# Performance work log

Hardware: AMD Instinct MI355X
Metric: run time of the kernel (lower is better)

## Reference

```python
import jax, jax.numpy as jnp
import numpy as np

Q7_MAX = 127.0  # int8 symmetric quant range
EPS = 1e-8


def setup_inputs() -> dict:
    key = jax.random.key(0)
    k0, k1, k2, k3 = jax.random.split(key, 4)
    tokens, d_in, d_out = 4096, 4096, 6144  # 32*128 + 8*128 + 8*128
    x = jax.random.normal(k0, (tokens, d_in), dtype=jnp.float32)
    # pre-quantized int8 weight [out_features, in_features]
    weight = jax.random.randint(k1, (d_out, d_in), -128, 128, dtype=jnp.int8)
    # per-output-channel dequant scale [out_features, 1]
    scale = jax.random.uniform(k2, (d_out, 1), dtype=jnp.float32, minval=1e-3, maxval=1e-2)
    bias = jax.random.normal(k3, (d_out,), dtype=jnp.float32) * 0.01
    return {"x": x, "weight": weight, "scale": scale, "bias": bias}


def reference(x, weight, scale, bias):
    # dynamic per-token symmetric int8 quantization of activations
    amax = jnp.max(jnp.abs(x), axis=-1, keepdims=True)          # [T, 1]
    s_x = jnp.maximum(amax, EPS) / Q7_MAX                        # per-token scale
    x_q = jnp.clip(jnp.round(x / s_x), -128.0, 127.0).astype(jnp.int8)
    acc = jnp.matmul(x_q.astype(jnp.int32), weight.astype(jnp.int32).T)
    # fused dequant: per-token act scale * per-channel weight scale, plus bias
    out = acc.astype(jnp.float32) * s_x * scale.T + bias
    return out
```

## Files before the change

kernel.cpp:

```cpp
#include <hip/hip_runtime.h>
#include <stdint.h>
#include <stddef.h>

typedef __attribute__((ext_vector_type(4))) int i32x4;

#define AS1q __attribute__((address_space(1)))
#define AS3q __attribute__((address_space(3)))

__device__ __forceinline__ void gload16(const void* g, void* l) {
    __builtin_amdgcn_global_load_lds((const AS1q uint32_t*)g, (AS3q uint32_t*)l, 16, 0, 0);
}

#define VMCNT(n)  asm volatile("s_waitcnt vmcnt(" #n ")" ::: "memory")
#define BARRIER() asm volatile("s_barrier" ::: "memory")

#define EPSQ 1e-8f

__global__ __launch_bounds__(256) void quant4096(
    const float* __restrict__ x, int8_t* __restrict__ xq, float* __restrict__ sx)
{
    constexpr int K = 4096;
    const int t = blockIdx.x;
    const int tid = threadIdx.x;
    const float4* row4 = (const float4*)(x + (size_t)t * K);
    float4 v0 = row4[0 * 256 + tid];
    float4 v1 = row4[1 * 256 + tid];
    float4 v2 = row4[2 * 256 + tid];
    float4 v3 = row4[3 * 256 + tid];
    auto mx4 = [](float4 a) {
        return fmaxf(fmaxf(fabsf(a.x), fabsf(a.y)), fmaxf(fabsf(a.z), fabsf(a.w)));
    };
    float am = fmaxf(fmaxf(mx4(v0), mx4(v1)), fmaxf(mx4(v2), mx4(v3)));
    #pragma unroll
    for (int off = 32; off > 0; off >>= 1)
        am = fmaxf(am, __shfl_xor(am, off, 64));
    __shared__ float wmax[4];
    if ((tid & 63) == 0) wmax[tid >> 6] = am;
    __syncthreads();
    float r = fmaxf(fmaxf(wmax[0], wmax[1]), fmaxf(wmax[2], wmax[3]));
    const float s = fmaxf(r, EPSQ) / 127.0f;
    if (tid == 0) sx[t] = s;
    int* qrow = (int*)(xq + (size_t)t * K);
    auto pack = [&](float4 a) {
        int q0 = (int)fminf(fmaxf(rintf(a.x / s), -128.f), 127.f);
        int q1 = (int)fminf(fmaxf(rintf(a.y / s), -128.f), 127.f);
        int q2 = (int)fminf(fmaxf(rintf(a.z / s), -128.f), 127.f);
        int q3 = (int)fminf(fmaxf(rintf(a.w / s), -128.f), 127.f);
        return (q0 & 255) | ((q1 & 255) << 8) | ((q2 & 255) << 16) | ((q3 & 255) << 24);
    };
    qrow[0 * 256 + tid] = pack(v0);
    qrow[1 * 256 + tid] = pack(v1);
    qrow[2 * 256 + tid] = pack(v2);
    qrow[3 * 256 + tid] = pack(v3);
}

__global__ __launch_bounds__(256) void quant_any(
    const float* __restrict__ x, int8_t* __restrict__ xq, float* __restrict__ sx, int K)
{
    const int t = blockIdx.x;
    const int tid = threadIdx.x;
    const float* row = x + (size_t)t * K;
    float am = 0.f;
    for (int i = tid; i < K; i += 256) am = fmaxf(am, fabsf(row[i]));
    #pragma unroll
    for (int off = 32; off > 0; off >>= 1)
        am = fmaxf(am, __shfl_xor(am, off, 64));
    __shared__ float wmax[4];
    if ((tid & 63) == 0) wmax[tid >> 6] = am;
    __syncthreads();
    float r = fmaxf(fmaxf(wmax[0], wmax[1]), fmaxf(wmax[2], wmax[3]));
    const float s = fmaxf(r, EPSQ) / 127.0f;
    if (tid == 0) sx[t] = s;
    int8_t* qrow = xq + (size_t)t * K;
    for (int i = tid; i < K; i += 256) {
        float q = fminf(fmaxf(rintf(row[i] / s), -128.f), 127.f);
        qrow[i] = (int8_t)(int)q;
    }
}

__global__ __launch_bounds__(256) void pack_w(
    const int* __restrict__ w32, int8_t* __restrict__ w8, long long n4)
{
    const long long stride = (long long)gridDim.x * 256;
    for (long long i = (long long)blockIdx.x * 256 + threadIdx.x; i < n4; i += stride) {
        int4 v = ((const int4*)w32)[i];
        ((int*)w8)[i] = (v.x & 255) | ((v.y & 255) << 8) | ((v.z & 255) << 16) | ((v.w & 255) << 24);
    }
}

__global__ __launch_bounds__(256, 2) void gemm_i8(
    const int8_t* __restrict__ xq, const int8_t* __restrict__ w,
    const float* __restrict__ sx, const float* __restrict__ scale,
    const float* __restrict__ bias, float* __restrict__ out,
    int M, int N, int K)
{
    __shared__ __align__(16) uint8_t lds[2][24576];
    const int tid  = threadIdx.x;
    const int lane = tid & 63;
    const int wv   = tid >> 6;
    const int wr   = wv >> 1, wc = wv & 1;

    const int nwg = gridDim.x;
    const int q8 = nwg >> 3, r8 = nwg & 7;
    const int xcd = blockIdx.x & 7, idx8 = blockIdx.x >> 3;
    const int wg = (xcd < r8 ? xcd * (q8 + 1) : r8 * (q8 + 1) + (xcd - r8) * q8) + idx8;

    const int NBM = M >> 8;
    const int bm = wg % NBM;
    const int bn = wg / NBM;
    const int brow = bm << 8, bcol = bn << 7;

    const int8_t* srcA[4];
    const int8_t* srcB[2];
    #pragma unroll
    for (int e = 0; e < 4; ++e) {
        int li = e * 256 + tid;
        int R  = li >> 3;
        int x  = ((li & 7) << 4) ^ ((R & 7) << 4);
        srcA[e] = xq + (size_t)(brow + ((R << 1) | (x >> 6))) * K + (x & 63);
    }
    #pragma unroll
    for (int e = 0; e < 2; ++e) {
        int li = e * 256 + tid;
        int R  = li >> 3;
        int x  = ((li & 7) << 4) ^ ((R & 7) << 4);
        srcB[e] = w + (size_t)(bcol + ((R << 1) | (x >> 6))) * K + (x & 63);
    }

    int offA[8], offB[4];
    #pragma unroll
    for (int m = 0; m < 8; ++m) {
        int r  = wr * 128 + m * 16 + (lane & 15);
        int R  = r >> 1;
        int x  = (((r & 1) << 6) | (lane & 48)) ^ ((R & 7) << 4);
        offA[m] = R * 128 + x;
    }
    #pragma unroll
    for (int n = 0; n < 4; ++n) {
        int r  = wc * 64 + n * 16 + (lane & 15);
        int R  = r >> 1;
        int x  = (((r & 1) << 6) | (lane & 48)) ^ ((R & 7) << 4);
        offB[n] = 16384 + R * 128 + x;
    }

    i32x4 acc[8][4] = {};

    auto stage = [&](int buf, int kt) {
        const size_t ko = (size_t)kt << 6;
        #pragma unroll
        for (int e = 0; e < 4; ++e)
            gload16(srcA[e] + ko, &lds[buf][e * 4096 + wv * 1024]);
        #pragma unroll
        for (int e = 0; e < 2; ++e)
            gload16(srcB[e] + ko, &lds[buf][16384 + e * 4096 + wv * 1024]);
    };

    const int NT = K >> 6;
    stage(0, 0);
    if (NT > 1) stage(1, 1);
    for (int kt = 0; kt < NT; ++kt) {
        if (kt < NT - 1) { VMCNT(6); } else { VMCNT(0); }
        BARRIER();
        const uint8_t* buf = lds[kt & 1];

        i32x4 av0[4], av1[4], bv[4];
        #pragma unroll
        for (int m = 0; m < 4; ++m) av0[m] = *(const i32x4*)(buf + offA[m]);
        #pragma unroll
        for (int n = 0; n < 4; ++n) bv[n] = *(const i32x4*)(buf + offB[n]);
        BARRIER();
        __builtin_amdgcn_s_setprio(1);
        #pragma unroll
        for (int m = 0; m < 4; ++m)
            #pragma unroll
            for (int n = 0; n < 4; ++n)
                acc[m][n] = __builtin_amdgcn_mfma_i32_16x16x64_i8(av0[m], bv[n], acc[m][n], 0, 0, 0);
        __builtin_amdgcn_s_setprio(0);
        #pragma unroll
        for (int m = 0; m < 4; ++m) av1[m] = *(const i32x4*)(buf + offA[4 + m]);
        BARRIER();
        __builtin_amdgcn_s_setprio(1);
        #pragma unroll
        for (int m = 0; m < 4; ++m)
            #pragma unroll
            for (int n = 0; n < 4; ++n)
                acc[4 + m][n] = __builtin_amdgcn_mfma_i32_16x16x64_i8(av1[m], bv[n], acc[4 + m][n], 0, 0, 0);
        __builtin_amdgcn_s_setprio(0);
        BARRIER();
        if (kt + 2 < NT) stage(kt & 1, kt + 2);
    }

    const int orow = brow + wr * 128;
    const int ocol = bcol + wc * 64;
    float sxv[8][4];
    #pragma unroll
    for (int m = 0; m < 8; ++m)
        #pragma unroll
        for (int j = 0; j < 4; ++j)
            sxv[m][j] = sx[orow + m * 16 + ((lane >> 4) << 2) + j];
    #pragma unroll
    for (int n = 0; n < 4; ++n) {
        const int col = ocol + n * 16 + (lane & 15);
        const float sc = scale[col];
        const float bi = bias[col];
        #pragma unroll
        for (int m = 0; m < 8; ++m) {
            const int rb = orow + m * 16 + ((lane >> 4) << 2);
            #pragma unroll
            for (int j = 0; j < 4; ++j)
                out[(size_t)(rb + j) * N + col] = (float)acc[m][n][j] * sxv[m][j] * sc + bi;
        }
    }
}

extern "C" void kernel_launch(void* const* d_in, const int* in_sizes, int n_in,
                              void* d_out, int out_size, void* d_ws, size_t ws_size,
                              hipStream_t stream) {
    const float* x     = (const float*)d_in[0];
    const int*   w32   = (const int*)d_in[1];
    const float* scale = (const float*)d_in[2];
    const float* bias  = (const float*)d_in[3];
    float* out = (float*)d_out;

    const int N = in_sizes[2];
    const int K = in_sizes[1] / N;
    const int M = in_sizes[0] / K;

    int8_t* xqbuf = (int8_t*)d_ws;
    int8_t* wqbuf = (int8_t*)d_ws + (size_t)M * K;
    float*  sxbuf = (float*)((uint8_t*)d_ws + (size_t)M * K + (size_t)N * K);

    if (K == 4096)
        quant4096<<<M, 256, 0, stream>>>(x, xqbuf, sxbuf);
    else
        quant_any<<<M, 256, 0, stream>>>(x, xqbuf, sxbuf, K);

    pack_w<<<2048, 256, 0, stream>>>(w32, wqbuf, (long long)N * K / 4);

    const int nwg = (M / 256) * (N / 128);
    gemm_i8<<<nwg, 256, 0, stream>>>(xqbuf, wqbuf, sxbuf, scale, bias, out, M, N, K);
}
```

Measured before the change: 161.0 us.

## Widen GEMM tile to 256x192, load B directly to registers, triple-buffer A

Grows the GEMM output tile from 256x128 to 256x192, so each wave owns 8x6 accumulator fragments and each A tile feeds more MFMAs. B fragments now go straight from global memory into registers, double-buffered across k-steps, instead of being staged through LDS. A uses a three-slot LDS ring with one barrier per iteration instead of four. The larger accumulator set forces occupancy to one workgroup per CU, and the per-lane B loads are strided 16-byte reads that may coalesce poorly.

Measured after the change: 256.1 us. +59.1%, slower.

```diff
diff --git a/kernel.cpp b/kernel.cpp
--- a/kernel.cpp
+++ b/kernel.cpp
@@ -88,13 +88,13 @@
     }
 }
 
-__global__ __launch_bounds__(256, 2) void gemm_i8(
+__global__ __launch_bounds__(256, 1) void gemm_i8(
     const int8_t* __restrict__ xq, const int8_t* __restrict__ w,
     const float* __restrict__ sx, const float* __restrict__ scale,
     const float* __restrict__ bias, float* __restrict__ out,
     int M, int N, int K)
 {
-    __shared__ __align__(16) uint8_t lds[2][24576];
+    __shared__ __align__(16) uint8_t lds[3][16384];
     const int tid  = threadIdx.x;
     const int lane = tid & 63;
     const int wv   = tid >> 6;
@@ -108,10 +108,9 @@
     const int NBM = M >> 8;
     const int bm = wg % NBM;
     const int bn = wg / NBM;
-    const int brow = bm << 8, bcol = bn << 7;
+    const int brow = bm << 8, bcol = bn * 192;
 
     const int8_t* srcA[4];
-    const int8_t* srcB[2];
     #pragma unroll
     for (int e = 0; e < 4; ++e) {
         int li = e * 256 + tid;
@@ -119,15 +118,8 @@
         int x  = ((li & 7) << 4) ^ ((R & 7) << 4);
         srcA[e] = xq + (size_t)(brow + ((R << 1) | (x >> 6))) * K + (x & 63);
     }
-    #pragma unroll
-    for (int e = 0; e < 2; ++e) {
-        int li = e * 256 + tid;
-        int R  = li >> 3;
-        int x  = ((li & 7) << 4) ^ ((R & 7) << 4);
-        srcB[e] = w + (size_t)(bcol + ((R << 1) | (x >> 6))) * K + (x & 63);
-    }
-
-    int offA[8], offB[4];
+
+    int offA[8];
     #pragma unroll
     for (int m = 0; m < 8; ++m) {
         int r  = wr * 128 + m * 16 + (lane & 15);
@@ -135,63 +127,63 @@
         int x  = (((r & 1) << 6) | (lane & 48)) ^ ((R & 7) << 4);
         offA[m] = R * 128 + x;
     }
-    #pragma unroll
-    for (int n = 0; n < 4; ++n) {
-        int r  = wc * 64 + n * 16 + (lane & 15);
-        int R  = r >> 1;
-        int x  = (((r & 1) << 6) | (lane & 48)) ^ ((R & 7) << 4);
-        offB[n] = 16384 + R * 128 + x;
-    }
-
-    i32x4 acc[8][4] = {};
-
-    auto stage = [&](int buf, int kt) {
+
+    const int8_t* bptr[6];
+    #pragma unroll
+    for (int n = 0; n < 6; ++n) {
+        const int col = bcol + wc * 96 + n * 16 + (lane & 15);
+        bptr[n] = w + (size_t)col * K + ((lane >> 4) << 4);
+    }
+
+    i32x4 acc[8][6] = {};
+
+    auto stageA = [&](int buf, int kt) {
         const size_t ko = (size_t)kt << 6;
         #pragma unroll
         for (int e = 0; e < 4; ++e)
             gload16(srcA[e] + ko, &lds[buf][e * 4096 + wv * 1024]);
-        #pragma unroll
-        for (int e = 0; e < 2; ++e)
-            gload16(srcB[e] + ko, &lds[buf][16384 + e * 4096 + wv * 1024]);
     };
 
     const int NT = K >> 6;
-    stage(0, 0);
-    if (NT > 1) stage(1, 1);
-    for (int kt = 0; kt < NT; ++kt) {
+    i32x4 bEven[6], bOdd[6];
+
+    stageA(0, 0);
+    if (NT > 1) stageA(1, 1);
+    #pragma unroll
+    for (int n = 0; n < 6; ++n) bEven[n] = *(const i32x4*)(bptr[n]);
+
+    auto body = [&](int kt, i32x4 (&bC)[6], i32x4 (&bN)[6]) {
         if (kt < NT - 1) { VMCNT(6); } else { VMCNT(0); }
         BARRIER();
-        const uint8_t* buf = lds[kt & 1];
-
-        i32x4 av0[4], av1[4], bv[4];
-        #pragma unroll
-        for (int m = 0; m < 4; ++m) av0[m] = *(const i32x4*)(buf + offA[m]);
-        #pragma unroll
-        for (int n = 0; n < 4; ++n) bv[n] = *(const i32x4*)(buf + offB[n]);
-        BARRIER();
+        if (kt + 1 < NT) {
+            const size_t ko = (size_t)(kt + 1) << 6;
+            #pragma unroll
+            for (int n = 0; n < 6; ++n) bN[n] = *(const i32x4*)(bptr[n] + ko);
+        }
+        if (kt + 2 < NT) {
+            int nb = kt + 2; nb -= (nb / 3) * 3;
+            stageA(nb, kt + 2);
+        }
+        const uint8_t* buf = lds[kt % 3];
+        i32x4 aF[8];
+        #pragma unroll
+        for (int m = 0; m < 8; ++m) aF[m] = *(const i32x4*)(buf + offA[m]);
         __builtin_amdgcn_s_setprio(1);
         #pragma unroll
-        for (int m = 0; m < 4; ++m)
+        for (int m = 0; m < 8; ++m)
             #pragma unroll
-            for (int n = 0; n < 4; ++n)
-                acc[m][n] = __builtin_amdgcn_mfma_i32_16x16x64_i8(av0[m], bv[n], acc[m][n], 0, 0, 0);
+            for (int n = 0; n < 6; ++n)
+                acc[m][n] = __builtin_amdgcn_mfma_i32_16x16x64_i8(aF[m], bC[n], acc[m][n], 0, 0, 0);
         __builtin_amdgcn_s_setprio(0);
-        #pragma unroll
-        for (int m = 0; m < 4; ++m) av1[m] = *(const i32x4*)(buf + offA[4 + m]);
-        BARRIER();
-        __builtin_amdgcn_s_setprio(1);
-        #pragma unroll
-        for (int m = 0; m < 4; ++m)
-            #pragma unroll
-            for (int n = 0; n < 4; ++n)
-                acc[4 + m][n] = __builtin_amdgcn_mfma_i32_16x16x64_i8(av1[m], bv[n], acc[4 + m][n], 0, 0, 0);
-        __builtin_amdgcn_s_setprio(0);
-        BARRIER();
-        if (kt + 2 < NT) stage(kt & 1, kt + 2);
+    };
+
+    for (int kt = 0; kt < NT; kt += 2) {
+        body(kt,     bEven, bOdd);
+        body(kt + 1, bOdd,  bEven);
     }
 
     const int orow = brow + wr * 128;
-    const int ocol = bcol + wc * 64;
+    const int ocol = bcol + wc * 96;
     float sxv[8][4];
     #pragma unroll
     for (int m = 0; m < 8; ++m)
@@ -199,7 +191,7 @@
         for (int j = 0; j < 4; ++j)
             sxv[m][j] = sx[orow + m * 16 + ((lane >> 4) << 2) + j];
     #pragma unroll
-    for (int n = 0; n < 4; ++n) {
+    for (int n = 0; n < 6; ++n) {
         const int col = ocol + n * 16 + (lane & 15);
         const float sc = scale[col];
         const float bi = bias[col];
@@ -237,6 +229,6 @@
 
     pack_w<<<2048, 256, 0, stream>>>(w32, wqbuf, (long long)N * K / 4);
 
-    const int nwg = (M / 256) * (N / 128);
+    const int nwg = (M / 256) * (N / 192);
     gemm_i8<<<nwg, 256, 0, stream>>>(xqbuf, wqbuf, sxbuf, scale, bias, out, M, N, K);
 }
```

## Enlarge GEMM tile to 256x256 with 8 waves and 4-deep half-tile pipeline

Applied to the files above, without the earlier changes.

The int8 GEMM block grows from 256x128 with 4 waves to 256x256 with 8 waves (512 threads), so each weight and activation byte staged into LDS is reused by more MFMAs. The K loop now streams 64-wide halves through a 2x2 LDS buffer (128 KB) with four stages in flight. Explicit vmcnt waits keep loads outstanding, and the next stage is issued in the middle of the MFMA sequence. LDS reads and MFMA quads are interleaved with barriers and setprio. The larger LDS footprint and 512-thread blocks reduce occupancy, and the extra barriers may add sync overhead.

Result: slower. 173.1 us (+7.5%).

```diff
diff --git a/kernel.cpp b/kernel.cpp
--- a/kernel.cpp
+++ b/kernel.cpp
@@ -11,8 +11,17 @@
     __builtin_amdgcn_global_load_lds((const AS1q uint32_t*)g, (AS3q uint32_t*)l, 16, 0, 0);
 }
 
-#define VMCNT(n)  asm volatile("s_waitcnt vmcnt(" #n ")" ::: "memory")
 #define BARRIER() asm volatile("s_barrier" ::: "memory")
+#define LGKMW()   do { asm volatile("s_waitcnt lgkmcnt(0)" ::: "memory"); \
+                       __builtin_amdgcn_sched_barrier(0); } while (0)
+
+template<int N> __device__ __forceinline__ void vmcnt_wait() {
+    if constexpr (N == 12)      asm volatile("s_waitcnt vmcnt(12)" ::: "memory");
+    else if constexpr (N == 8)  asm volatile("s_waitcnt vmcnt(8)"  ::: "memory");
+    else if constexpr (N == 4)  asm volatile("s_waitcnt vmcnt(4)"  ::: "memory");
+    else                        asm volatile("s_waitcnt vmcnt(0)"  ::: "memory");
+}
+template<int V> struct IC { static constexpr int v = V; };
 
 #define EPSQ 1e-8f
 
@@ -88,17 +97,30 @@
     }
 }
 
-__global__ __launch_bounds__(256, 2) void gemm_i8(
+#define MFMAI8(a, b, c) __builtin_amdgcn_mfma_i32_16x16x64_i8(a, b, c, 0, 0, 0)
+#define QUAD(MB, NB, A0, A1, A2, A3, B0, B1)                      \
+    __builtin_amdgcn_s_setprio(1);                                \
+    acc[MB+0][NB+0] = MFMAI8(A0, B0, acc[MB+0][NB+0]);            \
+    acc[MB+1][NB+0] = MFMAI8(A1, B0, acc[MB+1][NB+0]);            \
+    acc[MB+2][NB+0] = MFMAI8(A2, B0, acc[MB+2][NB+0]);            \
+    acc[MB+3][NB+0] = MFMAI8(A3, B0, acc[MB+3][NB+0]);            \
+    acc[MB+0][NB+1] = MFMAI8(A0, B1, acc[MB+0][NB+1]);            \
+    acc[MB+1][NB+1] = MFMAI8(A1, B1, acc[MB+1][NB+1]);            \
+    acc[MB+2][NB+1] = MFMAI8(A2, B1, acc[MB+2][NB+1]);            \
+    acc[MB+3][NB+1] = MFMAI8(A3, B1, acc[MB+3][NB+1]);            \
+    __builtin_amdgcn_s_setprio(0);
+
+__global__ __launch_bounds__(512, 2) void gemm_i8(
     const int8_t* __restrict__ xq, const int8_t* __restrict__ w,
     const float* __restrict__ sx, const float* __restrict__ scale,
     const float* __restrict__ bias, float* __restrict__ out,
     int M, int N, int K)
 {
-    __shared__ __align__(16) uint8_t lds[2][24576];
+    __shared__ __align__(16) uint8_t lds[2][2][32768];
     const int tid  = threadIdx.x;
     const int lane = tid & 63;
     const int wv   = tid >> 6;
-    const int wr   = wv >> 1, wc = wv & 1;
+    const int wr   = wv >> 2, wc = wv & 3;
 
     const int nwg = gridDim.x;
     const int q8 = nwg >> 3, r8 = nwg & 7;
@@ -108,23 +130,19 @@
     const int NBM = M >> 8;
     const int bm = wg % NBM;
     const int bn = wg / NBM;
-    const int brow = bm << 8, bcol = bn << 7;
-
-    const int8_t* srcA[4];
+    const int brow = bm << 8, bcol = bn << 8;
+
+    const int8_t* srcA[2];
     const int8_t* srcB[2];
     #pragma unroll
-    for (int e = 0; e < 4; ++e) {
-        int li = e * 256 + tid;
+    for (int e = 0; e < 2; ++e) {
+        int li = e * 512 + tid;
         int R  = li >> 3;
         int x  = ((li & 7) << 4) ^ ((R & 7) << 4);
-        srcA[e] = xq + (size_t)(brow + ((R << 1) | (x >> 6))) * K + (x & 63);
-    }
-    #pragma unroll
-    for (int e = 0; e < 2; ++e) {
-        int li = e * 256 + tid;
-        int R  = li >> 3;
-        int x  = ((li & 7) << 4) ^ ((R & 7) << 4);
-        srcB[e] = w + (size_t)(bcol + ((R << 1) | (x >> 6))) * K + (x & 63);
+        int r  = (R << 1) | (x >> 6);
+        int c  = x & 63;
+        srcA[e] = xq + (size_t)(brow + r) * K + c;
+        srcB[e] = w  + (size_t)(bcol + r) * K + c;
     }
 
     int offA[8], offB[4];
@@ -145,49 +163,64 @@
 
     i32x4 acc[8][4] = {};
 
-    auto stage = [&](int buf, int kt) {
-        const size_t ko = (size_t)kt << 6;
-        #pragma unroll
-        for (int e = 0; e < 4; ++e)
-            gload16(srcA[e] + ko, &lds[buf][e * 4096 + wv * 1024]);
-        #pragma unroll
-        for (int e = 0; e < 2; ++e)
-            gload16(srcB[e] + ko, &lds[buf][16384 + e * 4096 + wv * 1024]);
-    };
-
-    const int NT = K >> 6;
-    stage(0, 0);
-    if (NT > 1) stage(1, 1);
-    for (int kt = 0; kt < NT; ++kt) {
-        if (kt < NT - 1) { VMCNT(6); } else { VMCNT(0); }
-        BARRIER();
-        const uint8_t* buf = lds[kt & 1];
-
-        i32x4 av0[4], av1[4], bv[4];
-        #pragma unroll
-        for (int m = 0; m < 4; ++m) av0[m] = *(const i32x4*)(buf + offA[m]);
-        #pragma unroll
-        for (int n = 0; n < 4; ++n) bv[n] = *(const i32x4*)(buf + offB[n]);
-        BARRIER();
-        __builtin_amdgcn_s_setprio(1);
-        #pragma unroll
-        for (int m = 0; m < 4; ++m)
-            #pragma unroll
-            for (int n = 0; n < 4; ++n)
-                acc[m][n] = __builtin_amdgcn_mfma_i32_16x16x64_i8(av0[m], bv[n], acc[m][n], 0, 0, 0);
-        __builtin_amdgcn_s_setprio(0);
-        #pragma unroll
-        for (int m = 0; m < 4; ++m) av1[m] = *(const i32x4*)(buf + offA[4 + m]);
-        BARRIER();
-        __builtin_amdgcn_s_setprio(1);
-        #pragma unroll
-        for (int m = 0; m < 4; ++m)
-            #pragma unroll
-            for (int n = 0; n < 4; ++n)
-                acc[4 + m][n] = __builtin_amdgcn_mfma_i32_16x16x64_i8(av1[m], bv[n], acc[4 + m][n], 0, 0, 0);
-        __builtin_amdgcn_s_setprio(0);
-        BARRIER();
-        if (kt + 2 < NT) stage(kt & 1, kt + 2);
+    const int NT   = K >> 7;
+    const int hMax = NT * 2;
+
+    auto stageH = [&](int h) {
+        const int db = (h >> 1) & 1, hf = h & 1;
+        const size_t ko = (size_t)h << 6;
+        gload16(srcA[0] + ko, &lds[db][hf][wv * 1024]);
+        gload16(srcA[1] + ko, &lds[db][hf][8192  + wv * 1024]);
+        gload16(srcB[0] + ko, &lds[db][hf][16384 + wv * 1024]);
+        gload16(srcB[1] + ko, &lds[db][hf][24576 + wv * 1024]);
+    };
+
+    auto half4 = [&](const uint8_t* buf, int hS, auto Wc) {
+        i32x4 a0, a1, a2, a3, b0, b1, b2, b3;
+        a0 = *(const i32x4*)(buf + offA[0]);
+        a1 = *(const i32x4*)(buf + offA[1]);
+        a2 = *(const i32x4*)(buf + offA[2]);
+        a3 = *(const i32x4*)(buf + offA[3]);
+        b0 = *(const i32x4*)(buf + offB[0]);
+        b1 = *(const i32x4*)(buf + offB[1]);
+        BARRIER(); LGKMW();
+        QUAD(0, 0, a0, a1, a2, a3, b0, b1);
+        BARRIER();
+        b2 = *(const i32x4*)(buf + offB[2]);
+        b3 = *(const i32x4*)(buf + offB[3]);
+        BARRIER(); LGKMW();
+        QUAD(0, 2, a0, a1, a2, a3, b2, b3);
+        BARRIER();
+        a0 = *(const i32x4*)(buf + offA[4]);
+        a1 = *(const i32x4*)(buf + offA[5]);
+        a2 = *(const i32x4*)(buf + offA[6]);
+        a3 = *(const i32x4*)(buf + offA[7]);
+        BARRIER(); LGKMW();
+        QUAD(4, 0, a0, a1, a2, a3, b0, b1);
+        BARRIER();
+        if (hS < hMax) stageH(hS);
+        QUAD(4, 2, a0, a1, a2, a3, b2, b3);
+        vmcnt_wait<decltype(Wc)::v>();
+        BARRIER();
+    };
+
+    stageH(0); stageH(1); stageH(2); stageH(3);
+    vmcnt_wait<12>(); BARRIER();
+
+    for (int it = 0; it < NT - 2; ++it) {
+        const int db = it & 1;
+        half4(&lds[db][0][0], 2 * it + 4, IC<12>{});
+        half4(&lds[db][1][0], 2 * it + 5, IC<12>{});
+    }
+    {
+        const int db = (NT - 2) & 1;
+        half4(&lds[db][0][0], hMax, IC<8>{});
+        half4(&lds[db][1][0], hMax, IC<4>{});
+    }
+    {
+        const int db = (NT - 1) & 1;
+        half4(&lds[db][0][0], hMax, IC<0>{});
+        half4(&lds[db][1][0], hMax, IC<0>{});
     }
 
     const int orow = brow + wr * 128;
@@ -237,6 +270,6 @@
 
     pack_w<<<2048, 256, 0, stream>>>(w32, wqbuf, (long long)N * K / 4);
 
-    const int nwg = (M / 256) * (N / 128);
-    gemm_i8<<<nwg, 256, 0, stream>>>(xqbuf, wqbuf, sxbuf, scale, bias, out, M, N, K);
-}
+    const int nwg = (M / 256) * (N / 256);
+    gemm_i8<<<nwg, 512, 0, stream>>>(xqbuf, wqbuf, sxbuf, scale, bias, out, M, N, K);
+}
```

## Retile int8 GEMM to 128x192 with 4-stage LDS ring and register double-buffering

Applied to the files above, without the earlier changes.

Changes the GEMM block tile from 256x128 to 128x192, with each of the four waves owning a 128x48 column strip instead of a 2x2 wave grid. The shared-memory pipeline moves from two buffers to a four-deep ring with three tiles in flight. LDS fragment reads for the next k-step are ping-ponged in registers so they overlap the current MFMA batch, which also removes several barriers per iteration. The aim is better latency hiding and fewer sync stalls, at the cost of lower arithmetic intensity per tile (more A/B traffic per output) and more LDS and register use, which could reduce occupancy.

Result: slower. 169.4 us (+5.2%).

```diff
diff --git a/kernel.cpp b/kernel.cpp
--- a/kernel.cpp
+++ b/kernel.cpp
@@ -88,124 +88,131 @@
     }
 }
 
+#define MFMAI8(a, b, c) __builtin_amdgcn_mfma_i32_16x16x64_i8(a, b, c, 0, 0, 0)
+
 __global__ __launch_bounds__(256, 2) void gemm_i8(
     const int8_t* __restrict__ xq, const int8_t* __restrict__ w,
     const float* __restrict__ sx, const float* __restrict__ scale,
     const float* __restrict__ bias, float* __restrict__ out,
     int M, int N, int K)
 {
-    __shared__ __align__(16) uint8_t lds[2][24576];
+    __shared__ __align__(16) uint8_t lds[4][20480];
     const int tid  = threadIdx.x;
     const int lane = tid & 63;
     const int wv   = tid >> 6;
-    const int wr   = wv >> 1, wc = wv & 1;
+    const int wc   = wv;
 
     const int nwg = gridDim.x;
     const int q8 = nwg >> 3, r8 = nwg & 7;
     const int xcd = blockIdx.x & 7, idx8 = blockIdx.x >> 3;
     const int wg = (xcd < r8 ? xcd * (q8 + 1) : r8 * (q8 + 1) + (xcd - r8) * q8) + idx8;
 
-    const int NBM = M >> 8;
+    const int NBM = M >> 7;
     const int bm = wg % NBM;
     const int bn = wg / NBM;
-    const int brow = bm << 8, bcol = bn << 7;
-
-    const int8_t* srcA[4];
-    const int8_t* srcB[2];
-    #pragma unroll
-    for (int e = 0; e < 4; ++e) {
+    const int brow = bm << 7, bcol = bn * 192;
+
+    const int8_t* srcA[2];
+    const int8_t* srcB[3];
+    #pragma unroll
+    for (int e = 0; e < 2; ++e) {
         int li = e * 256 + tid;
         int R  = li >> 3;
         int x  = ((li & 7) << 4) ^ ((R & 7) << 4);
         srcA[e] = xq + (size_t)(brow + ((R << 1) | (x >> 6))) * K + (x & 63);
     }
     #pragma unroll
-    for (int e = 0; e < 2; ++e) {
+    for (int e = 0; e < 3; ++e) {
         int li = e * 256 + tid;
         int R  = li >> 3;
         int x  = ((li & 7) << 4) ^ ((R & 7) << 4);
         srcB[e] = w + (size_t)(bcol + ((R << 1) | (x >> 6))) * K + (x & 63);
     }
 
-    int offA[8], offB[4];
+    int offA[8], offB[3];
     #pragma unroll
     for (int m = 0; m < 8; ++m) {
-        int r  = wr * 128 + m * 16 + (lane & 15);
+        int r  = m * 16 + (lane & 15);
         int R  = r >> 1;
         int x  = (((r & 1) << 6) | (lane & 48)) ^ ((R & 7) << 4);
         offA[m] = R * 128 + x;
     }
     #pragma unroll
-    for (int n = 0; n < 4; ++n) {
-        int r  = wc * 64 + n * 16 + (lane & 15);
+    for (int n = 0; n < 3; ++n) {
+        int r  = wc * 48 + n * 16 + (lane & 15);
         int R  = r >> 1;
         int x  = (((r & 1) << 6) | (lane & 48)) ^ ((R & 7) << 4);
-        offB[n] = 16384 + R * 128 + x;
-    }
-
-    i32x4 acc[8][4] = {};
-
-    auto stage = [&](int buf, int kt) {
-        const size_t ko = (size_t)kt << 6;
-        #pragma unroll
-        for (int e = 0; e < 4; ++e)
-            gload16(srcA[e] + ko, &lds[buf][e * 4096 + wv * 1024]);
-        #pragma unroll
-        for (int e = 0; e < 2; ++e)
-            gload16(srcB[e] + ko, &lds[buf][16384 + e * 4096 + wv * 1024]);
-    };
-
-    const int NT = K >> 6;
-    stage(0, 0);
-    if (NT > 1) stage(1, 1);
-    for (int kt = 0; kt < NT; ++kt) {
-        if (kt < NT - 1) { VMCNT(6); } else { VMCNT(0); }
-        BARRIER();
-        const uint8_t* buf = lds[kt & 1];
-
-        i32x4 av0[4], av1[4], bv[4];
-        #pragma unroll
-        for (int m = 0; m < 4; ++m) av0[m] = *(const i32x4*)(buf + offA[m]);
-        #pragma unroll
-        for (int n = 0; n < 4; ++n) bv[n] = *(const i32x4*)(buf + offB[n]);
-        BARRIER();
+        offB[n] = 8192 + R * 128 + x;
+    }
+
+    i32x4 acc[8][3] = {};
+
+    auto stage = [&](int h) {
+        const int b = h & 3;
+        const size_t ko = (size_t)h << 6;
+        gload16(srcA[0] + ko, &lds[b][wv * 1024]);
+        gload16(srcA[1] + ko, &lds[b][4096 + wv * 1024]);
+        gload16(srcB[0] + ko, &lds[b][8192  + wv * 1024]);
+        gload16(srcB[1] + ko, &lds[b][12288 + wv * 1024]);
+        gload16(srcB[2] + ko, &lds[b][16384 + wv * 1024]);
+    };
+    auto readf = [&](int h, i32x4 (&fa)[8], i32x4 (&fb)[3]) {
+        const uint8_t* buf = lds[h & 3];
+        #pragma unroll
+        for (int m = 0; m < 8; ++m) fa[m] = *(const i32x4*)(buf + offA[m]);
+        #pragma unroll
+        for (int n = 0; n < 3; ++n) fb[n] = *(const i32x4*)(buf + offB[n]);
+    };
+    auto mfma24 = [&](i32x4 (&fa)[8], i32x4 (&fb)[3]) {
         __builtin_amdgcn_s_setprio(1);
         #pragma unroll
-        for (int m = 0; m < 4; ++m)
+        for (int m = 0; m < 8; ++m)
             #pragma unroll
-            for (int n = 0; n < 4; ++n)
-                acc[m][n] = __builtin_amdgcn_mfma_i32_16x16x64_i8(av0[m], bv[n], acc[m][n], 0, 0, 0);
+            for (int n = 0; n < 3; ++n)
+                acc[m][n] = MFMAI8(fa[m], fb[n], acc[m][n]);
         __builtin_amdgcn_s_setprio(0);
-        #pragma unroll
-        for (int m = 0; m < 4; ++m) av1[m] = *(const i32x4*)(buf + offA[4 + m]);
-        BARRIER();
-        __builtin_amdgcn_s_setprio(1);
-        #pragma unroll
-        for (int m = 0; m < 4; ++m)
-            #pragma unroll
-            for (int n = 0; n < 4; ++n)
-                acc[4 + m][n] = __builtin_amdgcn_mfma_i32_16x16x64_i8(av1[m], bv[n], acc[4 + m][n], 0, 0, 0);
-        __builtin_amdgcn_s_setprio(0);
-        BARRIER();
-        if (kt + 2 < NT) stage(kt & 1, kt + 2);
-    }
-
-    const int orow = brow + wr * 128;
-    const int ocol = bcol + wc * 64;
+    };
+
+    const int NH = K >> 6;
+    i32x4 fa0[8], fb0[3], fa1[8], fb1[3];
+
+    stage(0); stage(1); stage(2);
+    VMCNT(5); BARRIER();
+    readf(0, fa0, fb0);
+
+    for (int h = 0; h < NH; h += 2) {
+        if (h > 0) {
+            if (h < NH - 2) { VMCNT(5); } else { VMCNT(0); }
+            BARRIER();
+        }
+        if (h + 3 < NH) stage(h + 3);
+        if (h + 1 < NH) readf(h + 1, fa1, fb1);
+        mfma24(fa0, fb0);
+        {
+            const int g = h + 1;
+            if (g < NH - 2) { VMCNT(5); } else { VMCNT(0); }
+            BARRIER();
+            if (g + 3 < NH) stage(g + 3);
+            if (g + 1 < NH) readf(g + 1, fa0, fb0);
+            mfma24(fa1, fb1);
+        }
+    }
+
+    const int ocol = bcol + wc * 48;
     float sxv[8][4];
     #pragma unroll
     for (int m = 0; m < 8; ++m)
         #pragma unroll
         for (int j = 0; j < 4; ++j)
-            sxv[m][j] = sx[orow + m * 16 + ((lane >> 4) << 2) + j];
-    #pragma unroll
-    for (int n = 0; n < 4; ++n) {
+            sxv[m][j] = sx[brow + m * 16 + ((lane >> 4) << 2) + j];
+    #pragma unroll
+    for (int n = 0; n < 3; ++n) {
         const int col = ocol + n * 16 + (lane & 15);
         const float sc = scale[col];
         const float bi = bias[col];
         #pragma unroll
         for (int m = 0; m < 8; ++m) {
-            const int rb = orow + m * 16 + ((lane >> 4) << 2);
+            const int rb = brow + m * 16 + ((lane >> 4) << 2);
             #pragma unroll
             for (int j = 0; j < 4; ++j)
                 out[(size_t)(rb + j) * N + col] = (float)acc[m][n][j] * sxv[m][j] * sc + bi;
@@ -237,6 +244,6 @@
 
     pack_w<<<2048, 256, 0, stream>>>(w32, wqbuf, (long long)N * K / 4);
 
-    const int nwg = (M / 256) * (N / 128);
+    const int nwg = (M / 128) * (N / 192);
     gemm_i8<<<nwg, 256, 0, stream>>>(xqbuf, wqbuf, sxbuf, scale, bias, out, M, N, K);
 }
```
